# Kernel optimization log

Hardware: AMD Instinct MI355X
Metric: run time of the kernel (lower is better)

## Reference

```python
import jax, jax.numpy as jnp
import numpy as np

N = 10000      # num_nodes (also input feature width per GCNConv(num_nodes, 200))
E = 320000     # num edges (avg degree 32)
H1 = 200
C = 8
N_TEST = 2000


def _gcn_norm(edge_index, edge_weight, num_nodes):
    """PyG GCNConv symmetric normalization with self-loops (fill value 1)."""
    loop = jnp.arange(num_nodes)
    row = jnp.concatenate([edge_index[0], loop])          # source nodes
    col = jnp.concatenate([edge_index[1], loop])          # target nodes
    w = jnp.concatenate([edge_weight, jnp.ones((num_nodes,), edge_weight.dtype)])
    deg = jax.ops.segment_sum(w, col, num_segments=num_nodes)
    dis = jnp.where(deg > 0, jax.lax.rsqrt(deg), 0.0)     # deg^{-1/2}, 0 for isolated
    norm = dis[row] * w * dis[col]
    return row, col, norm


def _gcn_conv(x, row, col, norm, W, b, num_nodes):
    h = x @ W                                             # linear transform first (PyG order)
    msg = h[row] * norm[:, None]                          # gather + scale
    out = jax.ops.segment_sum(msg, col, num_segments=num_nodes)  # scatter-add aggregate
    return out + b


def setup_inputs() -> dict:
    key = jax.random.key(0)
    ks = jax.random.split(key, 8)
    x = jax.random.normal(ks[0], (N, N), jnp.float32)
    edge_index = jax.random.randint(ks[1], (2, E), 0, N, dtype=jnp.int64) if jax.config.read('jax_enable_x64') else jax.random.randint(ks[1], (2, E), 0, N)
    edge_weight = jax.random.uniform(ks[2], (E,), jnp.float32)
    mask_idx = jax.random.randint(ks[3], (N_TEST,), 0, N)
    y = jax.random.randint(ks[4], (N,), 0, C)
    W1 = jax.random.normal(ks[5], (N, H1), jnp.float32) / np.sqrt(N).astype(np.float32)
    b1 = jnp.zeros((H1,), jnp.float32)
    W2 = jax.random.normal(ks[6], (H1, C), jnp.float32) / np.sqrt(H1).astype(np.float32)
    b2 = jnp.zeros((C,), jnp.float32)
    return {"x": x, "edge_index": edge_index, "edge_weight": edge_weight,
            "mask_idx": mask_idx, "y": y, "W1": W1, "b1": b1, "W2": W2, "b2": b2}


def reference(x, edge_index, edge_weight, mask_idx, y, W1, b1, W2, b2):
    row, col, norm = _gcn_norm(edge_index, edge_weight, N)
    h = _gcn_conv(x, row, col, norm, W1, b1, N)
    h = jax.nn.relu(h)
    # dropout: module run in eval mode -> identity
    h = _gcn_conv(h, row, col, norm, W2, b2, N)
    predictions = h[mask_idx]   # masked gather (mode='test')
    targets = y[mask_idx]
    return predictions, targets
```

## Files before the change

kernel.cpp:

```cpp
#include <hip/hip_runtime.h>
#include <hip/hip_bf16.h>

#define NN     10000
#define NE     320000
#define H1DIM  200
#define H1BST  208
#define NCLS   8
#define NTST   2000
#define KDIM   10000
#define KPAD   10048
#define KSPL   6
#define KSTEPS 26
#define NGEMMB 474

typedef __bf16 bf16x8 __attribute__((ext_vector_type(8)));
typedef float  f32x4  __attribute__((ext_vector_type(4)));

__device__ __forceinline__ void load_lds16(const void* g, void* l) {
  __builtin_amdgcn_global_load_lds(
      (__attribute__((address_space(1))) void*)(void*)g,
      (__attribute__((address_space(3))) void*)l, 16, 0, 0);
}


__global__ void k_prep0(float* deg, int* cnt, int* cur, int* flags,
                        const unsigned* ei, const unsigned* mk, const unsigned* yy,
                        const float* __restrict__ W1, __bf16* __restrict__ Wt) {
  __shared__ float tile[64][65];
  __shared__ int s_f[4];
  int b = blockIdx.x, t = threadIdx.x;
  if (b < 40) {
    int i = b * 256 + t;
    if (i < NN) { deg[i] = 1.0f; cnt[i] = 0; cur[i] = 0; }
    return;
  }
  if (b < 43) {
    unsigned a = 0;
    if (b == 40)      { for (int i = t; i < 2048; i += 256) a |= ei[2 * i + 1]; }
    else if (b == 41) { for (int i = t; i < 2048; i += 256) a |= yy[2 * i + 1]; }
    else              { for (int i = t; i < 900;  i += 256) a |= mk[2 * i + 1]; }
    int wid = t >> 6;
    int any = __any(a != 0) ? 1 : 0;
    if ((t & 63) == 0) s_f[wid] = any;
    __syncthreads();
    if (t == 0) {
      int f = s_f[0] | s_f[1] | s_f[2] | s_f[3];
      int idx = (b == 40) ? 0 : (b == 41) ? 2 : 1;
      flags[idx] = f;
    }
    return;
  }
  int bt = b - 43;
  int k0 = (bt % 157) * 64, n0 = (bt / 157) * 64;
  int tn = t & 63, tk = t >> 6;
  for (int r = 0; r < 64; r += 4) {
    int k = k0 + tk + r, n = n0 + tn;
    tile[tk + r][tn] = (k < KDIM && n < H1DIM) ? W1[k * H1DIM + n] : 0.f;
  }
  __syncthreads();
  for (int r = 0; r < 64; r += 4) {
    int n = n0 + tk + r, k = k0 + tn;
    if (k < KPAD && n < 256)
      Wt[(size_t)n * KPAD + k] = (__bf16)tile[tn][tk + r];
  }
}


__global__ void k_gemm_cvt(const float* __restrict__ x, const __bf16* __restrict__ Wt,
                           __bf16* __restrict__ hpart,
                           const void* ei, const void* mk, const void* yy,
                           const float* __restrict__ ew, const int* __restrict__ flags,
                           int* idx32, int* mask32, int* y32, float* deg, int* cnt) {
  int t = threadIdx.x;
  if (blockIdx.x >= NGEMMB) {
    int i = (blockIdx.x - NGEMMB) * 512 + t;
    if (i < NE) {
      int v = (flags[0] == 0) ? (int)((const long long*)ei)[i] : ((const int*)ei)[i];
      idx32[i] = min(max(v, 0), NN - 1);
    } else if (i < 2 * NE) {
      int v = (flags[0] == 0) ? (int)((const long long*)ei)[i] : ((const int*)ei)[i];
      v = min(max(v, 0), NN - 1);
      idx32[i] = v;
      atomicAdd(&deg[v], ew[i - NE]);
      atomicAdd(&cnt[v], 1);
    } else if (i < 2 * NE + NTST) {
      int j = i - 2 * NE;
      int v = (flags[1] == 0) ? (int)((const long long*)mk)[j] : ((const int*)mk)[j];
      mask32[j] = min(max(v, 0), NN - 1);
    } else if (i < 2 * NE + NTST + NN) {
      int j = i - 2 * NE - NTST;
      int v = (flags[2] == 0) ? (int)((const long long*)yy)[j] : ((const int*)yy)[j];
      y32[j] = min(max(v, 0), NN - 1);
    }
    return;
  }

  __shared__ __align__(16) __bf16 As[128 * 64];
  __shared__ __align__(16) __bf16 Bs[256 * 64];
  int wv = t >> 6, lane = t & 63;
  int wm = wv >> 2, wn = wv & 3;
  int m0 = (blockIdx.x % 79) * 128;
  int split = blockIdx.x / 79;
  int kbeg = split * (KSTEPS * 64);
  int nsteps = KSTEPS + ((split == KSPL - 1) ? 1 : 0);

  f32x4 acc[4][4];
  #pragma unroll
  for (int i = 0; i < 4; ++i)
    #pragma unroll
    for (int j = 0; j < 4; ++j)
      #pragma unroll
      for (int r = 0; r < 4; ++r) acc[i][j][r] = 0.f;

  int am = t >> 2;
  int ac = t & 3;
  long arow = m0 + am; if (arow >= NN) arow = NN - 1;
  const float* aptr = x + (size_t)arow * KDIM + ac * 16;
  int ag0 = (2 * ac + 0) ^ (am & 7);
  int ag1 = (2 * ac + 1) ^ (am & 7);
  __bf16* awr0 = As + am * 64 + ag0 * 8;
  __bf16* awr1 = As + am * 64 + ag1 * 8;

  const __bf16* bsrc[4];
  __bf16* bdst[4];
  #pragma unroll
  for (int pass = 0; pass < 4; ++pass) {
    int s = pass * 512 + t;
    int brow = s >> 3, bg = s & 7;
    bsrc[pass] = Wt + (size_t)brow * KPAD + ((bg ^ (brow & 7)) * 8);
    bdst[pass] = Bs + (size_t)(pass * 512 + wv * 64) * 8;
  }

  int lrow = lane & 15;
  int lhi = lane >> 4;
  int lx7 = lane & 7;

  float4 v0, v1, v2, v3;
  {
    bool pr = (kbeg + ac * 16 + 16 <= KDIM);
    if (pr) {
      const float4* p = (const float4*)(aptr + kbeg);
      v0 = p[0]; v1 = p[1]; v2 = p[2]; v3 = p[3];
    }
  }

  for (int ks = 0; ks < nsteps; ++ks) {
    int k0 = kbeg + ks * 64;
    #pragma unroll
    for (int pass = 0; pass < 4; ++pass)
      load_lds16(bsrc[pass] + k0, bdst[pass]);
    {
      bool pr = (k0 + ac * 16 + 16 <= KDIM);
      bf16x8 bva, bvb;
      if (pr) {
        bva[0] = (__bf16)v0.x; bva[1] = (__bf16)v0.y;
        bva[2] = (__bf16)v0.z; bva[3] = (__bf16)v0.w;
        bva[4] = (__bf16)v1.x; bva[5] = (__bf16)v1.y;
        bva[6] = (__bf16)v1.z; bva[7] = (__bf16)v1.w;
        bvb[0] = (__bf16)v2.x; bvb[1] = (__bf16)v2.y;
        bvb[2] = (__bf16)v2.z; bvb[3] = (__bf16)v2.w;
        bvb[4] = (__bf16)v3.x; bvb[5] = (__bf16)v3.y;
        bvb[6] = (__bf16)v3.z; bvb[7] = (__bf16)v3.w;
      } else {
        #pragma unroll
        for (int q = 0; q < 8; ++q) { bva[q] = (__bf16)0.f; bvb[q] = (__bf16)0.f; }
      }
      *(bf16x8*)awr0 = bva;
      *(bf16x8*)awr1 = bvb;
    }
    __syncthreads();

    if (ks + 1 < nsteps) {
      int k1 = k0 + 64;
      bool pr = (k1 + ac * 16 + 16 <= KDIM);
      if (pr) {
        const float4* p = (const float4*)(aptr + k1);
        v0 = p[0]; v1 = p[1]; v2 = p[2]; v3 = p[3];
      }
    }

    #pragma unroll
    for (int kk = 0; kk < 2; ++kk) {
      int gs8 = ((kk * 4 + lhi) ^ lx7) * 8;
      bf16x8 af[4], bf[4];
      #pragma unroll
      for (int i = 0; i < 4; ++i)
        af[i] = *(const bf16x8*)&As[(wm * 64 + i * 16 + lrow) * 64 + gs8];
      #pragma unroll
      for (int j = 0; j < 4; ++j)
        bf[j] = *(const bf16x8*)&Bs[(wn * 64 + j * 16 + lrow) * 64 + gs8];
      #pragma unroll
      for (int i = 0; i < 4; ++i)
        #pragma unroll
        for (int j = 0; j < 4; ++j)
          acc[i][j] = __builtin_amdgcn_mfma_f32_16x16x32_bf16(af[i], bf[j], acc[i][j], 0, 0, 0);
    }
    __syncthreads();
  }

  __bf16* outp = hpart + (size_t)split * NN * H1BST;
  int colb = wn * 64 + (lane & 15);
  int rbase = m0 + wm * 64 + ((lane >> 4) * 4);
  #pragma unroll
  for (int i = 0; i < 4; ++i)
    #pragma unroll
    for (int j = 0; j < 4; ++j) {
      int cg = colb + j * 16;
      if (cg < H1BST) {
        #pragma unroll
        for (int r = 0; r < 4; ++r) {
          int rg = rbase + i * 16 + r;
          if (rg < NN) outp[(size_t)rg * H1BST + cg] = (__bf16)acc[i][j][r];
        }
      }
    }
}


__global__ void k_scan_red(const int* __restrict__ cnt, const float* __restrict__ deg,
                           float* dis, int* rowptr,
                           const __bf16* __restrict__ hpart, __bf16* __restrict__ h1b) {
  int t = threadIdx.x;
  if (blockIdx.x > 0) {
    int i = (blockIdx.x - 1) * 1024 + t;
    if (i < NN * 26) {
      int c = i / 26, ch = i - c * 26;
      size_t base = (size_t)c * H1BST + ch * 8;
      float s[8];
      #pragma unroll
      for (int q = 0; q < 8; ++q) s[q] = 0.f;
      #pragma unroll
      for (int sp = 0; sp < KSPL; ++sp) {
        bf16x8 v = *(const bf16x8*)(hpart + (size_t)sp * NN * H1BST + base);
        #pragma unroll
        for (int q = 0; q < 8; ++q) s[q] += (float)v[q];
      }
      bf16x8 o;
      #pragma unroll
      for (int q = 0; q < 8; ++q) o[q] = (__bf16)s[q];
      *(bf16x8*)&h1b[base] = o;
    }
    return;
  }
  __shared__ int wsum[16];
  __shared__ int carry;
  int lane = t & 63, wid = t >> 6;
  if (t == 0) carry = 0;
  __syncthreads();
  for (int base = 0; base < NN; base += 1024) {
    int idx = base + t;
    if (idx < NN) { float d = deg[idx]; dis[idx] = (d > 0.f) ? rsqrtf(d) : 0.f; }
    int v = (idx < NN) ? cnt[idx] : 0;
    int x = v;
    #pragma unroll
    for (int off = 1; off < 64; off <<= 1) {
      int y = __shfl_up(x, off);
      if (lane >= off) x += y;
    }
    if (lane == 63) wsum[wid] = x;
    __syncthreads();
    int c0 = carry;
    if (t < 16) {
      int s = wsum[t];
      #pragma unroll
      for (int off = 1; off < 16; off <<= 1) {
        int y = __shfl_up(s, off);
        if (t >= off) s += y;
      }
      wsum[t] = s;
    }
    __syncthreads();
    int woff = (wid == 0) ? 0 : wsum[wid - 1];
    if (idx < NN) rowptr[idx] = c0 + woff + x - v;
    int tot = wsum[15];
    __syncthreads();
    if (t == 0) carry = c0 + tot;
    __syncthreads();
  }
  if (t == 0) rowptr[NN] = carry;
}

__global__ void k_norm_scatter(const int* __restrict__ rows, const int* __restrict__ cols,
                               const float* __restrict__ w, const float* __restrict__ dis,
                               const int* __restrict__ rowptr, int* cur,
                               float* normv, int* eids) {
  int e = blockIdx.x * 512 + threadIdx.x;
  if (e < NE) {
    int r = rows[e], c = cols[e];
    normv[e] = dis[r] * w[e] * dis[c];
    int pos = rowptr[c] + atomicAdd(&cur[c], 1);
    eids[pos] = e;
  }
}


__global__ void k_agg1lin2(const __bf16* __restrict__ h1b, const float* __restrict__ dis,
                           const float* __restrict__ normv, const int* __restrict__ rows,
                           const int* __restrict__ rowptr, const int* __restrict__ eids,
                           const float* __restrict__ b1, const float* __restrict__ W2,
                           float* __restrict__ h2) {
  __shared__ int   s_r[512];
  __shared__ float s_n[512];
  __shared__ float s_p[4][8];
  int c = blockIdx.x;
  int t = threadIdx.x;
  int lane = t & 63, wid = t >> 6;
  int p0 = rowptr[c], len = rowptr[c + 1] - p0;
  float acc = 0.f;
  for (int base = 0; base < len; base += 512) {
    int chunk = min(512, len - base);
    for (int j = t; j < chunk; j += 256) {
      int e = eids[p0 + base + j];
      s_r[j] = rows[e];
      s_n[j] = normv[e];
    }
    __syncthreads();
    if (t < H1DIM) {
      int j = 0;
      for (; j + 4 <= chunk; j += 4) {
        float v0 = s_n[j + 0] * (float)h1b[(size_t)s_r[j + 0] * H1BST + t];
        float v1 = s_n[j + 1] * (float)h1b[(size_t)s_r[j + 1] * H1BST + t];
        float v2 = s_n[j + 2] * (float)h1b[(size_t)s_r[j + 2] * H1BST + t];
        float v3 = s_n[j + 3] * (float)h1b[(size_t)s_r[j + 3] * H1BST + t];
        acc += v0 + v1 + v2 + v3;
      }
      for (; j < chunk; ++j) acc += s_n[j] * (float)h1b[(size_t)s_r[j] * H1BST + t];
    }
    __syncthreads();
  }
  float a = 0.f;
  if (t < H1DIM) {
    float d = dis[c];
    a = acc + d * d * (float)h1b[(size_t)c * H1BST + t] + b1[t];
    a = fmaxf(a, 0.f);
  }
  float p[8];
  if (t < H1DIM) {
    float4 w2a = *(const float4*)&W2[t * 8];
    float4 w2b = *(const float4*)&W2[t * 8 + 4];
    p[0] = a * w2a.x; p[1] = a * w2a.y; p[2] = a * w2a.z; p[3] = a * w2a.w;
    p[4] = a * w2b.x; p[5] = a * w2b.y; p[6] = a * w2b.z; p[7] = a * w2b.w;
  } else {
    #pragma unroll
    for (int o = 0; o < 8; ++o) p[o] = 0.f;
  }
  #pragma unroll
  for (int s = 32; s >= 1; s >>= 1) {
    #pragma unroll
    for (int o = 0; o < 8; ++o) p[o] += __shfl_down(p[o], s);
  }
  if (lane == 0) {
    #pragma unroll
    for (int o = 0; o < 8; ++o) s_p[wid][o] = p[o];
  }
  __syncthreads();
  if (t < 8)
    h2[(size_t)c * 8 + t] = s_p[0][t] + s_p[1][t] + s_p[2][t] + s_p[3][t];
}


__global__ void k_agg2out(const float* __restrict__ h2, const float* __restrict__ dis,
                          const float* __restrict__ normv, const int* __restrict__ rows,
                          const int* __restrict__ rowptr, const int* __restrict__ eids,
                          const float* __restrict__ b2, const int* __restrict__ mask,
                          const int* __restrict__ yv, float* __restrict__ out) {
  int i = blockIdx.x * 256 + threadIdx.x;
  if (i < NTST * NCLS) {
    int r = i >> 3, o = i & 7;
    int c = mask[r];
    float d = dis[c];
    float acc = d * d * h2[c * NCLS + o];
    int p0 = rowptr[c], p1 = rowptr[c + 1];
    for (int j = p0; j < p1; ++j) {
      int e = eids[j];
      acc += normv[e] * h2[rows[e] * NCLS + o];
    }
    out[i] = acc + b2[o];
  } else if (i < NTST * NCLS + NTST) {
    int r = i - NTST * NCLS;
    out[i] = (float)yv[mask[r]];
  }
}


extern "C" void kernel_launch(void* const* d_in, const int* in_sizes, int n_in,
                              void* d_out, int out_size, void* d_ws, size_t ws_size,
                              hipStream_t stream) {
  const float* x    = (const float*)d_in[0];
  const void*  ei   = d_in[1];
  const float* ew   = (const float*)d_in[2];
  const void*  mask = d_in[3];
  const void*  y    = d_in[4];
  const float* W1   = (const float*)d_in[5];
  const float* b1   = (const float*)d_in[6];
  const float* W2   = (const float*)d_in[7];
  const float* b2   = (const float*)d_in[8];
  float* out = (float*)d_out;

  char* ws = (char*)d_ws;
  float* deg    = (float*)(ws + 0);
  float* dis    = (float*)(ws + (64 << 10));
  float* normv  = (float*)(ws + (128 << 10));
  int*   idx32  = (int*)(ws + (2 << 20));
  float* h2     = (float*)(ws + (5 << 20));
  int*   mask32 = (int*)(ws + (6 << 20));
  int*   y32    = (int*)(ws + (6 << 20) + (64 << 10));
  int*   flags  = (int*)(ws + (6 << 20) + (128 << 10));
  int*   cnt    = (int*)(ws + (6 << 20) + (256 << 10));
  int*   cur    = (int*)(ws + (6 << 20) + (384 << 10));
  int*   rowptr = (int*)(ws + (6 << 20) + (512 << 10));
  int*   eids   = (int*)(ws + (7 << 20));
  __bf16* Wt    = (__bf16*)(ws + ((size_t)9 << 20));
  __bf16* h1b   = (__bf16*)(ws + ((size_t)16 << 20));
  __bf16* hpart = (__bf16*)(ws + ((size_t)24 << 20));

  int* rows32 = idx32;
  int* cols32 = idx32 + NE;

  k_prep0<<<dim3(671), dim3(256), 0, stream>>>(deg, cnt, cur, flags,
                                               (const unsigned*)ei, (const unsigned*)mask,
                                               (const unsigned*)y, W1, Wt);

  k_gemm_cvt<<<dim3(NGEMMB + 1274), dim3(512), 0, stream>>>(
      x, Wt, hpart, ei, mask, y, ew, flags, idx32, mask32, y32, deg, cnt);

  k_scan_red<<<dim3(255), dim3(1024), 0, stream>>>(cnt, deg, dis, rowptr, hpart, h1b);

  k_norm_scatter<<<dim3(625), dim3(512), 0, stream>>>(rows32, cols32, ew, dis, rowptr, cur,
                                                      normv, eids);

  k_agg1lin2<<<dim3(10000), dim3(256), 0, stream>>>(h1b, dis, normv, rows32, rowptr, eids,
                                                    b1, W2, h2);
  k_agg2out<<<dim3(71), dim3(256), 0, stream>>>(h2, dis, normv, rows32, rowptr, eids, b2,
                                                mask32, y32, out);
}
```

Baseline: 255.1 us.

## Widen GEMM A-tile K depth to 128 with two B sub-stages per step

The split-K bf16 GEMM now converts and stores a 128-wide K slice of x into LDS per outer step, with a 16-way XOR swizzle, and loads the B tile twice per step (two 64-wide halves). This halves the number of outer iterations and the A-conversion barriers, and doubles the register prefetch depth for the fp32 x stream. KPAD and the W1 transpose grid are enlarged to cover the new K padding. In exchange, the A tile needs more LDS, more registers are used for prefetch, and extra syncs are added around the second B load, which may lower occupancy.

After: 492.0 us. 92.9% more time.

```diff
diff --git a/kernel.cpp b/kernel.cpp
--- a/kernel.cpp
+++ b/kernel.cpp
@@ -8,9 +8,9 @@
 #define NCLS   8
 #define NTST   2000
 #define KDIM   10000
-#define KPAD   10048
+#define KPAD   10112
 #define KSPL   6
-#define KSTEPS 26
+#define KSTEPS 13
 #define NGEMMB 474
 
 typedef __bf16 bf16x8 __attribute__((ext_vector_type(8)));
@@ -51,7 +51,7 @@
     return;
   }
   int bt = b - 43;
-  int k0 = (bt % 157) * 64, n0 = (bt / 157) * 64;
+  int k0 = (bt % 158) * 64, n0 = (bt / 158) * 64;
   int tn = t & 63, tk = t >> 6;
   for (int r = 0; r < 64; r += 4) {
     int k = k0 + tk + r, n = n0 + tn;
@@ -95,13 +95,13 @@
     return;
   }
 
-  __shared__ __align__(16) __bf16 As[128 * 64];
+  __shared__ __align__(16) __bf16 As[128 * 128];
   __shared__ __align__(16) __bf16 Bs[256 * 64];
   int wv = t >> 6, lane = t & 63;
   int wm = wv >> 2, wn = wv & 3;
   int m0 = (blockIdx.x % 79) * 128;
   int split = blockIdx.x / 79;
-  int kbeg = split * (KSTEPS * 64);
+  int kbeg = split * (KSTEPS * 128);
   int nsteps = KSTEPS + ((split == KSPL - 1) ? 1 : 0);
 
   f32x4 acc[4][4];
@@ -115,11 +115,7 @@
   int am = t >> 2;
   int ac = t & 3;
   long arow = m0 + am; if (arow >= NN) arow = NN - 1;
-  const float* aptr = x + (size_t)arow * KDIM + ac * 16;
-  int ag0 = (2 * ac + 0) ^ (am & 7);
-  int ag1 = (2 * ac + 1) ^ (am & 7);
-  __bf16* awr0 = As + am * 64 + ag0 * 8;
-  __bf16* awr1 = As + am * 64 + ag1 * 8;
+  const float* aptr = x + (size_t)arow * KDIM + ac * 32;
 
   const __bf16* bsrc[4];
   __bf16* bdst[4];
@@ -135,60 +131,80 @@
   int lhi = lane >> 4;
   int lx7 = lane & 7;
 
-  float4 v0, v1, v2, v3;
-  {
-    bool pr = (kbeg + ac * 16 + 16 <= KDIM);
-    if (pr) {
-      const float4* p = (const float4*)(aptr + kbeg);
-      v0 = p[0]; v1 = p[1]; v2 = p[2]; v3 = p[3];
-    }
-  }
+  float4 v[8];
+  #define PREFA(kq)                                                        \
+    do {                                                                   \
+      if ((kq) + 128 <= KDIM) {                                            \
+        const float4* p = (const float4*)(aptr + (kq));                    \
+        _Pragma("unroll")                                                  \
+        for (int j = 0; j < 8; ++j) v[j] = p[j];                           \
+      } else {                                                             \
+        _Pragma("unroll")                                                  \
+        for (int j = 0; j < 8; ++j) {                                      \
+          if ((kq) + ac * 32 + j * 4 + 4 <= KDIM)                          \
+            v[j] = *(const float4*)(aptr + (kq) + j * 4);                  \
+          else { v[j].x = 0.f; v[j].y = 0.f; v[j].z = 0.f; v[j].w = 0.f; } \
+        }                                                                  \
+      }                                                                    \
+    } while (0)
+
+  PREFA(kbeg);
 
   for (int ks = 0; ks < nsteps; ++ks) {
-    int k0 = kbeg + ks * 64;
+    int k0 = kbeg + ks * 128;
     #pragma unroll
     for (int pass = 0; pass < 4; ++pass)
       load_lds16(bsrc[pass] + k0, bdst[pass]);
-    {
-      bool pr = (k0 + ac * 16 + 16 <= KDIM);
-      bf16x8 bva, bvb;
-      if (pr) {
-        bva[0] = (__bf16)v0.x; bva[1] = (__bf16)v0.y;
-        bva[2] = (__bf16)v0.z; bva[3] = (__bf16)v0.w;
-        bva[4] = (__bf16)v1.x; bva[5] = (__bf16)v1.y;
-        bva[6] = (__bf16)v1.z; bva[7] = (__bf16)v1.w;
-        bvb[0] = (__bf16)v2.x; bvb[1] = (__bf16)v2.y;
-        bvb[2] = (__bf16)v2.z; bvb[3] = (__bf16)v2.w;
-        bvb[4] = (__bf16)v3.x; bvb[5] = (__bf16)v3.y;
-        bvb[6] = (__bf16)v3.z; bvb[7] = (__bf16)v3.w;
-      } else {
+    #pragma unroll
+    for (int j = 0; j < 4; ++j) {
+      bf16x8 bv;
+      float4 a0 = v[2 * j], a1 = v[2 * j + 1];
+      bv[0] = (__bf16)a0.x; bv[1] = (__bf16)a0.y;
+      bv[2] = (__bf16)a0.z; bv[3] = (__bf16)a0.w;
+      bv[4] = (__bf16)a1.x; bv[5] = (__bf16)a1.y;
+      bv[6] = (__bf16)a1.z; bv[7] = (__bf16)a1.w;
+      int g = (ac * 4 + j) ^ (am & 15);
+      *(bf16x8*)(As + am * 128 + g * 8) = bv;
+    }
+    __syncthreads();
+
+    if (ks + 1 < nsteps) { int k1 = k0 + 128; PREFA(k1); }
+
+    #pragma unroll
+    for (int kk = 0; kk < 2; ++kk) {
+      int gA = ((kk * 4 + lhi) ^ lrow) * 8;
+      int gB = ((kk * 4 + lhi) ^ lx7) * 8;
+      bf16x8 af[4], bf[4];
+      #pragma unroll
+      for (int i = 0; i < 4; ++i)
+        af[i] = *(const bf16x8*)&As[(wm * 64 + i * 16 + lrow) * 128 + gA];
+      #pragma unroll
+      for (int j = 0; j < 4; ++j)
+        bf[j] = *(const bf16x8*)&Bs[(wn * 64 + j * 16 + lrow) * 64 + gB];
+      #pragma unroll
+      for (int i = 0; i < 4; ++i)
         #pragma unroll
-        for (int q = 0; q < 8; ++q) { bva[q] = (__bf16)0.f; bvb[q] = (__bf16)0.f; }
-      }
-      *(bf16x8*)awr0 = bva;
-      *(bf16x8*)awr1 = bvb;
-    }
-    __syncthreads();
-
-    if (ks + 1 < nsteps) {
-      int k1 = k0 + 64;
-      bool pr = (k1 + ac * 16 + 16 <= KDIM);
-      if (pr) {
-        const float4* p = (const float4*)(aptr + k1);
-        v0 = p[0]; v1 = p[1]; v2 = p[2]; v3 = p[3];
-      }
-    }
+        for (int j = 0; j < 4; ++j)
+          acc[i][j] = __builtin_amdgcn_mfma_f32_16x16x32_bf16(af[i], bf[j], acc[i][j], 0, 0, 0);
+    }
+    __syncthreads();
+
+    #pragma unroll
+    for (int pass = 0; pass < 4; ++pass)
+      load_lds16(bsrc[pass] + k0 + 64, bdst[pass]);
+    __syncthreads();
 
     #pragma unroll
     for (int kk = 0; kk < 2; ++kk) {
-      int gs8 = ((kk * 4 + lhi) ^ lx7) * 8;
+      int gA = (((kk + 2) * 4 + lhi) ^ lrow) * 8;
+      int gB = ((kk * 4 + lhi) ^ lx7) * 8;
       bf16x8 af[4], bf[4];
       #pragma unroll
       for (int i = 0; i < 4; ++i)
-        af[i] = *(const bf16x8*)&As[(wm * 64 + i * 16 + lrow) * 64 + gs8];
+        af[i] = *(const bf16x8*)&As[(wm * 64 + i * 16 + lrow) * 128 + gA];
       #pragma unroll
       for (int j = 0; j < 4; ++j)
-        bf[j] = *(const bf16x8*)&Bs[(wn * 64 + j * 16 + lrow) * 64 + gs8];
+        bf[j] = *(const bf16x8*)&Bs[(wn * 64 + j * 16 + lrow) * 64 + gB];
       #pragma unroll
       for (int i = 0; i < 4; ++i)
         #pragma unroll
@@ -417,7 +433,7 @@
   int* rows32 = idx32;
   int* cols32 = idx32 + NE;
 
-  k_prep0<<<dim3(671), dim3(256), 0, stream>>>(deg, cnt, cur, flags,
+  k_prep0<<<dim3(675), dim3(256), 0, stream>>>(deg, cnt, cur, flags,
                                                (const unsigned*)ei, (const unsigned*)mask,
                                                (const unsigned*)y, W1, Wt);
 
```
